# Performance work log

Measured on AMD Instinct MI355X. Metric: run time of the kernel, lower is better.

## Reference

```python
import jax, jax.numpy as jnp
import numpy as np

NEG_SLOPE = 0.01
EPS = 1e-5


def leaky_relu(x):
    return jnp.where(x >= 0, x, NEG_SLOPE * x)


def graph_conv(x, W, src, dst, edge_weight, num_nodes):
    # DGL GraphConv, norm='both', bias=False: D_out^{-1/2} A_w D_in^{-1/2} X W
    ones = jnp.ones_like(edge_weight)
    deg_out = jnp.maximum(jax.ops.segment_sum(ones, src, num_segments=num_nodes), 1.0)
    deg_in = jnp.maximum(jax.ops.segment_sum(ones, dst, num_segments=num_nodes), 1.0)
    h = x @ W
    h = h * jax.lax.rsqrt(deg_out)[:, None]
    agg = jax.ops.segment_sum(h[src] * edge_weight[:, None], dst, num_segments=num_nodes)
    return agg * jax.lax.rsqrt(deg_in)[:, None]


def graph_norm(x, alpha, gamma, beta, batch_size):
    # GraphNorm: per-graph, per-channel mean/var; graphs are equal-sized -> reshape
    n = x.shape[0] // batch_size
    xg = x.reshape(batch_size, n, x.shape[1])
    mean = xg.mean(axis=1, keepdims=True)
    sub = xg - alpha * mean
    var = (sub * sub).mean(axis=1, keepdims=True)
    out = gamma * sub * jax.lax.rsqrt(var + EPS) + beta
    return out.reshape(x.shape)


def instance_norm(x):
    # InstanceNorm1d (affine=False) on 2D input: per-row normalization over features
    mean = x.mean(axis=-1, keepdims=True)
    var = ((x - mean) ** 2).mean(axis=-1, keepdims=True)
    return (x - mean) * jax.lax.rsqrt(var + EPS)


def setup_inputs() -> dict:
    key = jax.random.key(0)
    ks = jax.random.split(key, 9)
    B, n = 4096, 64                      # graphs, nodes per graph (equal-sized)
    N = B * n                            # 262144 nodes
    E = 8 * N                            # avg degree 8
    in_feats, conv_dim, out_conv = 64, 128, 96
    in_mlp = out_conv * n                # 6144 = in_feats_mlp
    hid = 2048
    out_feats = 256

    def kaiming(k, fin, fout):
        bound = float(np.sqrt(6.0 / ((1 + NEG_SLOPE ** 2) * fin)))
        return jax.random.uniform(k, (fin, fout), jnp.float32, -bound, bound)

    def xavier(k, fin, fout):
        bound = float(np.sqrt(6.0 / (fin + fout)))
        return jax.random.uniform(k, (fin, fout), jnp.float32, -bound, bound)

    return {
        "x": jax.random.normal(ks[0], (N, in_feats), jnp.float32),
        "edge_weight": jax.random.uniform(ks[1], (E,), jnp.float32),
        "src": jax.random.randint(ks[2], (E,), 0, N, jnp.int32),
        "dst": jax.random.randint(ks[3], (E,), 0, N, jnp.int32),
        "W1": kaiming(ks[4], in_feats, conv_dim),
        "W2": kaiming(ks[5], conv_dim, out_conv),
        "gn1_alpha": jnp.ones((conv_dim,), jnp.float32),
        "gn1_gamma": jnp.ones((conv_dim,), jnp.float32),
        "gn1_beta": jnp.zeros((conv_dim,), jnp.float32),
        "gn2_alpha": jnp.ones((out_conv,), jnp.float32),
        "gn2_gamma": jnp.ones((out_conv,), jnp.float32),
        "gn2_beta": jnp.zeros((out_conv,), jnp.float32),
        "Win": xavier(ks[6], in_mlp, hid),
        "Whid": xavier(ks[7], hid, hid // 4),
        "Wcls": xavier(ks[8], hid // 4, out_feats),
        "batch_size": B,
    }


def reference(x, edge_weight, src, dst, W1, W2, gn1_alpha, gn1_gamma, gn1_beta,
              gn2_alpha, gn2_gamma, gn2_beta, Win, Whid, Wcls, batch_size):
    N = x.shape[0]
    h = graph_conv(x, W1, src, dst, edge_weight, N)
    h = leaky_relu(h)
    h = graph_norm(h, gn1_alpha, gn1_gamma, gn1_beta, batch_size)
    h = graph_conv(h, W2, src, dst, edge_weight, N)
    h = leaky_relu(h)
    h = graph_norm(h, gn2_alpha, gn2_gamma, gn2_beta, batch_size)
    # unbatch: each equal-size graph flattened to one row [B, n*out_conv]
    h = h.reshape(batch_size, -1)
    h = instance_norm(leaky_relu(h @ Win))   # dropout is identity (p=0 / eval)
    h = instance_norm(leaky_relu(h @ Whid))
    return h @ Wcls
```

## Files before the change

kernel.cpp:

```cpp
#include <hip/hip_runtime.h>
#include <hip/hip_bf16.h>

#define NN 262144
#define EE 2097152
#define BB 4096
constexpr int INMLP = 6144;
constexpr int HID = 2048;
constexpr int HID4 = 512;
constexpr int OUTF = 256;
constexpr int NSL = 64;
constexpr int ESL = EE / NSL;
constexpr int RNODES = 32768;

typedef short s16x8 __attribute__((ext_vector_type(8)));
typedef short s16x4 __attribute__((ext_vector_type(4)));
typedef float f32x4 __attribute__((ext_vector_type(4)));

__device__ __forceinline__ float lrelu(float v) { return v >= 0.f ? v : 0.01f * v; }
__device__ __forceinline__ float bf2f(short s) {
    unsigned int u = ((unsigned int)(unsigned short)s) << 16;
    return __builtin_bit_cast(float, u);
}
__device__ __forceinline__ short f2bf(float f) {
    unsigned int u = __builtin_bit_cast(unsigned int, f);
    u = (u + 0x7fff + ((u >> 16) & 1)) >> 16;
    return (short)u;
}
__device__ __forceinline__ void async16(const void* g, void* l) {
    __builtin_amdgcn_global_load_lds((__attribute__((address_space(1))) void*)g,
                                     (__attribute__((address_space(3))) void*)l, 16, 0, 0);
}

__global__ __launch_bounds__(256) void hist_count(const int* __restrict__ dst, const int* __restrict__ src,
                                                  unsigned* __restrict__ part_din, unsigned* __restrict__ part_dout,
                                                  unsigned short* __restrict__ rankpack16) {
    __shared__ unsigned hist[RNODES / 2];
    const int S = blockIdx.x & 63;
    const int R = (blockIdx.x >> 6) & 7;
    const int T = blockIdx.x >> 9;
    for (int i = threadIdx.x; i < RNODES / 2; i += 256) hist[i] = 0;
    __syncthreads();
    const int* idxarr = T ? src : dst;
    const int4* v4 = (const int4*)(idxarr + S * ESL);
#pragma unroll 4
    for (int i = 0; i < ESL / 4 / 256; i++) {
        const int q0 = i * 256 + threadIdx.x;
        int4 q = v4[q0];
        const int ebase = S * ESL + q0 * 4;
#pragma unroll
        for (int k = 0; k < 4; k++) {
            int idx = k == 0 ? q.x : k == 1 ? q.y : k == 2 ? q.z : q.w;
            if ((idx >> 15) == R) {
                int local = idx & (RNODES - 1);
                unsigned old = atomicAdd(&hist[local >> 1], 1u << ((local & 1) * 16));
                if (T == 0) {
                    unsigned rank = (old >> ((local & 1) * 16)) & 0xffffu;
                    rankpack16[ebase + k] = (unsigned short)((S << 10) | rank);
                }
            }
        }
    }
    __syncthreads();
    unsigned* dp = (T ? part_dout : part_din) + (size_t)S * (NN / 2) + R * (RNODES / 2);
    for (int i = threadIdx.x; i < RNODES / 2; i += 256) dp[i] = hist[i];
}

__global__ __launch_bounds__(256) void deg_reduce(const unsigned* __restrict__ part_din,
                                                  const unsigned* __restrict__ part_dout,
                                                  unsigned* __restrict__ repbase_w,
                                                  float* __restrict__ ro, float* __restrict__ ri,
                                                  int* __restrict__ din) {
    int i = blockIdx.x * 256 + threadIdx.x;
    unsigned runl = 0, runh = 0, dl = 0, dh = 0;
#pragma unroll 8
    for (int S = 0; S < NSL; S++) {
        repbase_w[(size_t)S * (NN / 2) + i] = (runl & 0xffffu) | (runh << 16);
        unsigned w = part_din[(size_t)S * (NN / 2) + i];
        runl += w & 0xffffu; runh += w >> 16;
        unsigned w2 = part_dout[(size_t)S * (NN / 2) + i];
        dl += w2 & 0xffffu; dh += w2 >> 16;
    }
    int n0 = 2 * i, n1 = 2 * i + 1;
    din[n0] = (int)runl; din[n1] = (int)runh;
    ro[n0] = rsqrtf((float)(dl < 1u ? 1u : dl));
    ro[n1] = rsqrtf((float)(dh < 1u ? 1u : dh));
    ri[n0] = rsqrtf((float)(runl < 1u ? 1u : runl));
    ri[n1] = rsqrtf((float)(runh < 1u ? 1u : runh));
}

__global__ __launch_bounds__(256) void scanA(const int* __restrict__ cnt, int* __restrict__ blks) {
    __shared__ int s[256];
    int t = threadIdx.x;
    int i0 = blockIdx.x * 1024 + t * 4;
    int ts = cnt[i0] + cnt[i0 + 1] + cnt[i0 + 2] + cnt[i0 + 3];
    s[t] = ts; __syncthreads();
    for (int d = 128; d > 0; d >>= 1) { if (t < d) s[t] += s[t + d]; __syncthreads(); }
    if (t == 0) blks[blockIdx.x] = s[0];
}

__global__ __launch_bounds__(256) void scanB(int* __restrict__ blks, int* __restrict__ offN) {
    __shared__ int s[256];
    int t = threadIdx.x;
    int v = blks[t]; s[t] = v; __syncthreads();
    for (int d = 1; d < 256; d <<= 1) {
        int x = (t >= d) ? s[t - d] : 0; __syncthreads();
        s[t] += x; __syncthreads();
    }
    blks[t] = s[t] - v;
    if (t == 255) *offN = s[255];
}

__global__ __launch_bounds__(256) void scanC(const int* __restrict__ cnt, const int* __restrict__ blkoff,
                                             int* __restrict__ off) {
    __shared__ int s[256];
    int t = threadIdx.x;
    int i0 = blockIdx.x * 1024 + t * 4;
    int v0 = cnt[i0], v1 = cnt[i0 + 1], v2 = cnt[i0 + 2], v3 = cnt[i0 + 3];
    int ts = v0 + v1 + v2 + v3;
    s[t] = ts; __syncthreads();
    for (int d = 1; d < 256; d <<= 1) {
        int x = (t >= d) ? s[t - d] : 0; __syncthreads();
        s[t] += x; __syncthreads();
    }
    int base = blkoff[blockIdx.x] + (s[t] - ts);
    off[i0] = base; off[i0 + 1] = base + v0; off[i0 + 2] = base + v0 + v1; off[i0 + 3] = base + v0 + v1 + v2;
}

__global__ __launch_bounds__(256) void fill_csr(const int* __restrict__ src, const int* __restrict__ dst,
                                                const float* __restrict__ ew, const float* __restrict__ ro,
                                                const int* __restrict__ off,
                                                const unsigned short* __restrict__ repbase16,
                                                const unsigned short* __restrict__ rankpack16,
                                                int2* __restrict__ edg) {
    int e = blockIdx.x * 256 + threadIdx.x;
    int d = dst[e];
    int s = src[e];
    unsigned pk = rankpack16[e];
    int S = pk >> 10, rank = pk & 1023;
    int p = off[d] + (int)repbase16[(size_t)S * NN + d] + rank;
    edg[p] = make_int2(s, __builtin_bit_cast(int, ew[e] * ro[s]));
}

__global__ __launch_bounds__(256) void cvt_x(const float* __restrict__ X, short* __restrict__ Xb) {
    int i = (blockIdx.x * 256 + threadIdx.x) * 4;
    float4 v = *(const float4*)(X + i);
    s16x4 o = { f2bf(v.x), f2bf(v.y), f2bf(v.z), f2bf(v.w) };
    *(s16x4*)(Xb + i) = o;
}

__global__ __launch_bounds__(256) void gather64(const short* __restrict__ Xb, const int* __restrict__ offs,
                                                const int2* __restrict__ edg, short* __restrict__ Out) {
    const int lane = threadIdx.x & 63;
    const int e = lane >> 3, c = lane & 7;
    int node = blockIdx.x * 4 + (threadIdx.x >> 6);
    node = __builtin_amdgcn_readfirstlane(node);
    const int s0 = offs[node], s1 = offs[node + 1];
    float acc[8] = {};
    for (int j0 = s0; j0 < s1; j0 += 8) {
        int j = j0 + e;
        bool ok = j < s1;
        int2 pe = edg[ok ? j : s0];
        int s = pe.x;
        float w = ok ? __builtin_bit_cast(float, pe.y) : 0.f;
        s16x8 v = *(const s16x8*)&Xb[(size_t)s * 64 + c * 8];
#pragma unroll
        for (int k = 0; k < 8; k++) acc[k] = fmaf(w, bf2f(v[k]), acc[k]);
    }
#pragma unroll
    for (int off = 8; off <= 32; off <<= 1)
#pragma unroll
        for (int k = 0; k < 8; k++) acc[k] += __shfl_xor(acc[k], off);
    if (e == 0) {
        s16x8 o;
#pragma unroll
        for (int k = 0; k < 8; k++) o[k] = f2bf(acc[k]);
        *(s16x8*)&Out[(size_t)node * 64 + c * 8] = o;
    }
}

__global__ __launch_bounds__(256) void gather96(const short* __restrict__ H, const int* __restrict__ offs,
                                                const int2* __restrict__ edg, short* __restrict__ Out) {
    const int lane = threadIdx.x & 63;
    const int e = lane >> 4, c = lane & 15;
    int node = blockIdx.x * 4 + (threadIdx.x >> 6);
    node = __builtin_amdgcn_readfirstlane(node);
    const int s0 = offs[node], s1 = offs[node + 1];
    float acc[6] = {};
    for (int j0 = s0; j0 < s1; j0 += 4) {
        int j = j0 + e;
        bool ok = j < s1;
        int2 pe = edg[ok ? j : s0];
        int s = pe.x;
        float w = ok ? __builtin_bit_cast(float, pe.y) : 0.f;
        const unsigned int* hp = (const unsigned int*)(H + (size_t)s * 96 + c * 6);
        unsigned int u0 = hp[0], u1 = hp[1], u2 = hp[2];
        acc[0] = fmaf(w, bf2f((short)(u0 & 0xffff)), acc[0]);
        acc[1] = fmaf(w, bf2f((short)(u0 >> 16)), acc[1]);
        acc[2] = fmaf(w, bf2f((short)(u1 & 0xffff)), acc[2]);
        acc[3] = fmaf(w, bf2f((short)(u1 >> 16)), acc[3]);
        acc[4] = fmaf(w, bf2f((short)(u2 & 0xffff)), acc[4]);
        acc[5] = fmaf(w, bf2f((short)(u2 >> 16)), acc[5]);
    }
#pragma unroll
    for (int off = 16; off <= 32; off <<= 1)
#pragma unroll
        for (int k = 0; k < 6; k++) acc[k] += __shfl_xor(acc[k], off);
    if (e == 0) {
        unsigned int* op = (unsigned int*)(Out + (size_t)node * 96 + c * 6);
        op[0] = (unsigned short)f2bf(acc[0]) | ((unsigned)(unsigned short)f2bf(acc[1]) << 16);
        op[1] = (unsigned short)f2bf(acc[2]) | ((unsigned)(unsigned short)f2bf(acc[3]) << 16);
        op[2] = (unsigned short)f2bf(acc[4]) | ((unsigned)(unsigned short)f2bf(acc[5]) << 16);
    }
}

template <int C>
__global__ __launch_bounds__(256) void graphnorm_k(short* __restrict__ Ag, const float* __restrict__ ri,
                                                   const float* __restrict__ alpha, const float* __restrict__ gamma,
                                                   const float* __restrict__ beta) {
    __shared__ float sm[64 * C];
    __shared__ float sscale[C], sshift[C];
    const int g = blockIdx.x;
    const size_t base = (size_t)g * 64 * C;
    for (int idx = threadIdx.x; idx < 64 * C; idx += 256) {
        int i = idx / C;
        float v = bf2f(Ag[base + idx]) * ri[g * 64 + i];
        sm[idx] = lrelu(v);
    }
    __syncthreads();
    if (threadIdx.x < C) {
        int c = threadIdx.x;
        float s1 = 0.f, s2 = 0.f;
#pragma unroll 4
        for (int i = 0; i < 64; i++) { float v = sm[i * C + c]; s1 += v; s2 += v * v; }
        float m = s1 * (1.f / 64.f);
        float a = alpha[c];
        float var = s2 * (1.f / 64.f) - m * m * a * (2.f - a);
        float sc = gamma[c] * rsqrtf(var + 1e-5f);
        sscale[c] = sc;
        sshift[c] = beta[c] - sc * a * m;
    }
    __syncthreads();
    for (int idx = threadIdx.x; idx < 64 * C; idx += 256) {
        int c = idx % C;
        Ag[base + idx] = f2bf(sscale[c] * sm[idx] + sshift[c]);
    }
}

__global__ __launch_bounds__(256) void conv1_gn(const short* __restrict__ A, const short* __restrict__ BT,
                                                const float* __restrict__ ri,
                                                const float* __restrict__ alpha, const float* __restrict__ gamma,
                                                const float* __restrict__ beta, short* __restrict__ Outp) {
    __shared__ short As[128][72];
    __shared__ short Bs[128][72];
    __shared__ float sscale[2][128], sshift[2][128];
    const int t = threadIdx.x;
    const int bm = blockIdx.x * 128;
    const int wave = t >> 6, lane = t & 63;
    const int wm = (wave & 1) * 64, wn = (wave >> 1) * 64;
    const int g = wave & 1;
    const int m16 = lane & 15, quad = lane >> 4;
#pragma unroll
    for (int i = 0; i < 4; i++) {
        int idx = t + 256 * i;
        int rr = idx >> 3, kk = (idx & 7) * 8;
        *(s16x8*)&As[rr][kk] = *(const s16x8*)&A[(size_t)(bm + rr) * 64 + kk];
        *(s16x8*)&Bs[rr][kk] = *(const s16x8*)&BT[(size_t)rr * 64 + kk];
    }
    __syncthreads();
    f32x4 acc[4][4] = {};
#pragma unroll
    for (int kc = 0; kc < 2; kc++) {
        s16x8 af[4], bfr[4];
#pragma unroll
        for (int mt = 0; mt < 4; mt++) af[mt] = *(const s16x8*)&As[wm + mt * 16 + m16][kc * 32 + quad * 8];
#pragma unroll
        for (int nt = 0; nt < 4; nt++) bfr[nt] = *(const s16x8*)&Bs[wn + nt * 16 + m16][kc * 32 + quad * 8];
#pragma unroll
        for (int mt = 0; mt < 4; mt++)
#pragma unroll
            for (int nt = 0; nt < 4; nt++)
                acc[mt][nt] = __builtin_amdgcn_mfma_f32_16x16x32_bf16(af[mt], bfr[nt], acc[mt][nt], 0, 0, 0);
    }
#pragma unroll
    for (int mt = 0; mt < 4; mt++)
#pragma unroll
        for (int r4 = 0; r4 < 4; r4++) {
            float rv = ri[bm + wm + mt * 16 + quad * 4 + r4];
#pragma unroll
            for (int nt = 0; nt < 4; nt++)
                acc[mt][nt][r4] = lrelu(acc[mt][nt][r4] * rv);
        }
#pragma unroll
    for (int nt = 0; nt < 4; nt++) {
        float s1 = 0.f, s2 = 0.f;
#pragma unroll
        for (int mt = 0; mt < 4; mt++)
#pragma unroll
            for (int r4 = 0; r4 < 4; r4++) { float v = acc[mt][nt][r4]; s1 += v; s2 += v * v; }
        s1 += __shfl_xor(s1, 16); s1 += __shfl_xor(s1, 32);
        s2 += __shfl_xor(s2, 16); s2 += __shfl_xor(s2, 32);
        if (quad == 0) {
            int ch = wn + nt * 16 + m16;
            float m = s1 * (1.f / 64.f);
            float a = alpha[ch];
            float var = s2 * (1.f / 64.f) - m * m * a * (2.f - a);
            float sc = gamma[ch] * rsqrtf(var + 1e-5f);
            sscale[g][ch] = sc;
            sshift[g][ch] = beta[ch] - sc * a * m;
        }
    }
    __syncthreads();
#pragma unroll
    for (int nt = 0; nt < 4; nt++) {
        int ch = wn + nt * 16 + m16;
        float sc = sscale[g][ch], sh = sshift[g][ch];
#pragma unroll
        for (int mt = 0; mt < 4; mt++)
#pragma unroll
            for (int r4 = 0; r4 < 4; r4++) {
                int row = bm + wm + mt * 16 + quad * 4 + r4;
                Outp[(size_t)row * 128 + ch] = f2bf(sc * acc[mt][nt][r4] + sh);
            }
    }
}

__global__ __launch_bounds__(256) void conv2_mfma(const short* __restrict__ A, const short* __restrict__ BT,
                                                  short* __restrict__ H) {
    __shared__ short As[128][136];
    __shared__ short Bs[96][136];
    const int t = threadIdx.x;
    const int bm = blockIdx.x * 128;
    const int wave = t >> 6, lane = t & 63;
    const int wm = (wave & 1) * 64, wn = (wave >> 1) * 48;
    const int m16 = lane & 15, quad = lane >> 4;
#pragma unroll
    for (int i = 0; i < 8; i++) {
        int idx = t + 256 * i;
        int rr = idx >> 4, kk = (idx & 15) * 8;
        *(s16x8*)&As[rr][kk] = *(const s16x8*)&A[(size_t)(bm + rr) * 128 + kk];
    }
#pragma unroll
    for (int i = 0; i < 6; i++) {
        int idx = t + 256 * i;
        int nr = idx >> 4, kk = (idx & 15) * 8;
        *(s16x8*)&Bs[nr][kk] = *(const s16x8*)&BT[(size_t)nr * 128 + kk];
    }
    __syncthreads();
    f32x4 acc[4][3] = {};
#pragma unroll
    for (int kc = 0; kc < 4; kc++) {
        s16x8 af[4], bfr[3];
#pragma unroll
        for (int mt = 0; mt < 4; mt++) af[mt] = *(const s16x8*)&As[wm + mt * 16 + m16][kc * 32 + quad * 8];
#pragma unroll
        for (int nt = 0; nt < 3; nt++) bfr[nt] = *(const s16x8*)&Bs[wn + nt * 16 + m16][kc * 32 + quad * 8];
#pragma unroll
        for (int mt = 0; mt < 4; mt++)
#pragma unroll
            for (int nt = 0; nt < 3; nt++)
                acc[mt][nt] = __builtin_amdgcn_mfma_f32_16x16x32_bf16(af[mt], bfr[nt], acc[mt][nt], 0, 0, 0);
    }
#pragma unroll
    for (int mt = 0; mt < 4; mt++)
#pragma unroll
        for (int r4 = 0; r4 < 4; r4++) {
            int row = bm + wm + mt * 16 + quad * 4 + r4;
#pragma unroll
            for (int nt = 0; nt < 3; nt++)
                H[(size_t)row * 96 + wn + nt * 16 + m16] = f2bf(acc[mt][nt][r4]);
        }
}

__global__ __launch_bounds__(256) void transp_cvt(const float* __restrict__ W, short* __restrict__ WT,
                                                  int R, int Cc) {
    __shared__ short tile[32][33];
    const int bc = blockIdx.x * 32;
    const int br = blockIdx.y * 32;
    const int tx = threadIdx.x & 31, ty = threadIdx.x >> 5;
#pragma unroll
    for (int i = 0; i < 32; i += 8)
        tile[ty + i][tx] = f2bf(W[(size_t)(br + ty + i) * Cc + bc + tx]);
    __syncthreads();
#pragma unroll
    for (int i = 0; i < 32; i += 8)
        WT[(size_t)(bc + ty + i) * R + br + tx] = tile[tx][ty + i];
}

#define MBAR() __builtin_amdgcn_s_barrier()
#define LGKM0() asm volatile("s_waitcnt lgkmcnt(0)" ::: "memory")
#define SB0() __builtin_amdgcn_sched_barrier(0)

__global__ __launch_bounds__(512, 2) void mlp1_mfma8(const short* __restrict__ A, const short* __restrict__ BT,
                                                     short* __restrict__ Cp) {
    constexpr int K = INMLP;
    __shared__ short As[2][256 * 64];
    __shared__ short Bs[2][256 * 64];
    const int t = threadIdx.x;
    const int wid = t >> 6, lane = t & 63;
    const int lrow = lane >> 3, lcol = lane & 7;
    const int scol = lcol ^ (lrow & 7);
    const int m16 = lane & 15, quad = lane >> 4, xkey = m16 & 7;
    const int wm = wid & 1, wn = wid >> 1;
    const int sw = (blockIdx.x & 7) * 32 + (blockIdx.x >> 3);
    const int bm = sw & 15, bn = (sw >> 4) & 7, z = sw >> 7;
    const short* gA = A + (size_t)(bm * 256 + wid * 32 + lrow) * K + (size_t)z * (K / 2) + scol * 8;
    const short* gB = BT + (size_t)(bn * 256 + wid * 16 + lrow) * K + (size_t)z * (K / 2) + scol * 8;

    s16x8 a0[8], a1[8], b0[4], b1[4];
    f32x4 acc[8][4] = {};

#define STAGE_A(s, ko) \
    { _Pragma("unroll") for (int j = 0; j < 4; j++) \
        async16(gA + (size_t)(j * 8) * K + (ko), &As[s][(wid * 32 + j * 8) * 64]); }
#define STAGE_B(s, ko, h) \
    { _Pragma("unroll") for (int j = 0; j < 2; j++) \
        async16(gB + (size_t)((h) * 128 + j * 8) * K + (ko), &Bs[s][((h) * 128 + wid * 16 + j * 8) * 64]); }
#define LD_A(s, kc, d) \
    { _Pragma("unroll") for (int mt = 0; mt < 8; mt++) \
        d[mt] = *(const s16x8*)&As[s][(wm * 128 + mt * 16 + m16) * 64 + (((kc) * 4 + quad) ^ xkey) * 8]; }
#define LD_B(s, kc, d) \
    { _Pragma("unroll") for (int nt = 0; nt < 4; nt++) \
        d[nt] = *(const s16x8*)&Bs[s][(wn * 64 + nt * 16 + m16) * 64 + (((kc) * 4 + quad) ^ xkey) * 8]; }
#define MM2(a, b, nlo) \
    { _Pragma("unroll") for (int mt = 0; mt < 8; mt++) { \
        acc[mt][(nlo)] = __builtin_amdgcn_mfma_f32_16x16x32_bf16(a[mt], b[(nlo)], acc[mt][(nlo)], 0, 0, 0); \
        acc[mt][(nlo) + 1] = __builtin_amdgcn_mfma_f32_16x16x32_bf16(a[mt], b[(nlo) + 1], acc[mt][(nlo) + 1], 0, 0, 0); } }

    STAGE_A(0, 0); STAGE_B(0, 0, 0); STAGE_B(0, 0, 1);
    STAGE_B(1, 64, 0); STAGE_B(1, 64, 1); STAGE_A(1, 64);
    asm volatile("s_waitcnt vmcnt(8)" ::: "memory");
    MBAR();

    int kof = 0;
#pragma unroll 1
    for (int i = 0; i < 24; i++, kof += 128) {
        const bool st = (i < 23);
        LD_A(0, 0, a0); LD_B(0, 0, b0);
        MBAR(); LGKM0(); SB0();
        __builtin_amdgcn_s_setprio(1); MM2(a0, b0, 0); __builtin_amdgcn_s_setprio(0);
        MBAR();
        LD_A(0, 1, a1); LD_B(0, 1, b1);
        MBAR(); LGKM0(); SB0();
        __builtin_amdgcn_s_setprio(1); MM2(a0, b0, 2); __builtin_amdgcn_s_setprio(0);
        MBAR();
        if (st) STAGE_A(0, kof + 128);
        MBAR(); LGKM0(); SB0();
        __builtin_amdgcn_s_setprio(1); MM2(a1, b1, 0); __builtin_amdgcn_s_setprio(0);
        if (st) { asm volatile("s_waitcnt vmcnt(4)" ::: "memory"); }
        else    { asm volatile("s_waitcnt vmcnt(0)" ::: "memory"); }
        MBAR();
        LD_A(1, 0, a0); LD_B(1, 0, b0);
        if (st) STAGE_B(0, kof + 128, 0);
        MBAR(); LGKM0(); SB0();
        __builtin_amdgcn_s_setprio(1); MM2(a1, b1, 2); __builtin_amdgcn_s_setprio(0);
        MBAR();
        LD_A(1, 1, a1); LD_B(1, 1, b1);
        if (st) STAGE_B(0, kof + 128, 1);
        MBAR(); LGKM0(); SB0();
        __builtin_amdgcn_s_setprio(1); MM2(a0, b0, 0); __builtin_amdgcn_s_setprio(0);
        MBAR();
        if (st) STAGE_B(1, kof + 192, 0);
        MBAR(); LGKM0(); SB0();
        __builtin_amdgcn_s_setprio(1); MM2(a0, b0, 2); __builtin_amdgcn_s_setprio(0);
        MBAR();
        if (st) STAGE_B(1, kof + 192, 1);
        MBAR(); LGKM0(); SB0();
        __builtin_amdgcn_s_setprio(1); MM2(a1, b1, 0); __builtin_amdgcn_s_setprio(0);
        MBAR();
        if (st) STAGE_A(1, kof + 192);
        MBAR(); LGKM0(); SB0();
        __builtin_amdgcn_s_setprio(1); MM2(a1, b1, 2); __builtin_amdgcn_s_setprio(0);
        if (st) { asm volatile("s_waitcnt vmcnt(8)" ::: "memory"); }
        MBAR();
    }

    short* C = Cp + (size_t)z * BB * HID;
    const int r0 = bm * 256 + wm * 128 + quad * 4;
    const int c0 = bn * 256 + wn * 64 + m16;
#pragma unroll
    for (int mt = 0; mt < 8; mt++)
#pragma unroll
        for (int nt = 0; nt < 4; nt++)
#pragma unroll
            for (int r4 = 0; r4 < 4; r4++)
                C[(size_t)(r0 + mt * 16 + r4) * HID + c0 + nt * 16] = f2bf(acc[mt][nt][r4]);
#undef STAGE_A
#undef STAGE_B
#undef LD_A
#undef LD_B
#undef MM2
}

__global__ __launch_bounds__(256) void rownorm_hid(short* __restrict__ D0, const short* __restrict__ D1) {
    const size_t base = (size_t)blockIdx.x * HID;
    float v[8];
    float s1 = 0.f, s2 = 0.f;
    const int c0 = threadIdx.x * 8;
    {
        s16x8 a = *(const s16x8*)&D0[base + c0];
        s16x8 b = *(const s16x8*)&D1[base + c0];
#pragma unroll
        for (int k = 0; k < 8; k++) {
            float x = lrelu(bf2f(a[k]) + bf2f(b[k]));
            v[k] = x; s1 += x; s2 += x * x;
        }
    }
#pragma unroll
    for (int o = 32; o > 0; o >>= 1) { s1 += __shfl_down(s1, o); s2 += __shfl_down(s2, o); }
    __shared__ float w1[4], w2[4];
    if ((threadIdx.x & 63) == 0) { w1[threadIdx.x >> 6] = s1; w2[threadIdx.x >> 6] = s2; }
    __syncthreads();
    s1 = w1[0] + w1[1] + w1[2] + w1[3];
    s2 = w2[0] + w2[1] + w2[2] + w2[3];
    float m = s1 * (1.f / HID);
    float inv = rsqrtf(s2 * (1.f / HID) - m * m + 1e-5f);
    s16x8 o;
#pragma unroll
    for (int k = 0; k < 8; k++) o[k] = f2bf((v[k] - m) * inv);
    *(s16x8*)&D0[base + c0] = o;
}

template <bool ABF16, bool LEAKY>
__global__ __launch_bounds__(256) void mfma_gemm(const float* __restrict__ Af, const short* __restrict__ Ab,
                                                 const short* __restrict__ BT,
                                                 float* __restrict__ C, int M, int Nn, int K) {
    __shared__ short As[64][40];
    __shared__ short Bs[64][40];
    const int t = threadIdx.x;
    const int bm = blockIdx.x * 64, bn = blockIdx.y * 64;
    const int wave = t >> 6, lane = t & 63;
    const int wm = (wave & 1) * 32, wn = (wave >> 1) * 32;
    const int m16 = lane & 15, quad = lane >> 4;
    const int rr = t >> 2, kk = (t & 3) * 8;
    f32x4 acc[2][2] = {};
    for (int k0 = 0; k0 < K; k0 += 32) {
        if (ABF16) {
            *(s16x8*)&As[rr][kk] = *(const s16x8*)&Ab[(size_t)(bm + rr) * K + k0 + kk];
        } else {
            const float* ap = &Af[(size_t)(bm + rr) * K + k0 + kk];
            float4 v0 = *(const float4*)ap;
            float4 v1 = *(const float4*)(ap + 4);
            s16x8 a8;
            a8[0] = f2bf(v0.x); a8[1] = f2bf(v0.y); a8[2] = f2bf(v0.z); a8[3] = f2bf(v0.w);
            a8[4] = f2bf(v1.x); a8[5] = f2bf(v1.y); a8[6] = f2bf(v1.z); a8[7] = f2bf(v1.w);
            *(s16x8*)&As[rr][kk] = a8;
        }
        *(s16x8*)&Bs[rr][kk] = *(const s16x8*)&BT[(size_t)(bn + rr) * K + k0 + kk];
        __syncthreads();
        s16x8 af[2], bfr[2];
#pragma unroll
        for (int mt = 0; mt < 2; mt++) af[mt] = *(const s16x8*)&As[wm + mt * 16 + m16][quad * 8];
#pragma unroll
        for (int nt = 0; nt < 2; nt++) bfr[nt] = *(const s16x8*)&Bs[wn + nt * 16 + m16][quad * 8];
#pragma unroll
        for (int mt = 0; mt < 2; mt++)
#pragma unroll
            for (int nt = 0; nt < 2; nt++)
                acc[mt][nt] = __builtin_amdgcn_mfma_f32_16x16x32_bf16(af[mt], bfr[nt], acc[mt][nt], 0, 0, 0);
        __syncthreads();
    }
#pragma unroll
    for (int mt = 0; mt < 2; mt++)
#pragma unroll
        for (int nt = 0; nt < 2; nt++)
#pragma unroll
            for (int r4 = 0; r4 < 4; r4++) {
                int row = bm + wm + mt * 16 + quad * 4 + r4;
                int col = bn + wn + nt * 16 + m16;
                float v = acc[mt][nt][r4];
                if (LEAKY) v = lrelu(v);
                C[(size_t)row * Nn + col] = v;
            }
}

template <int NC>
__global__ __launch_bounds__(256) void rownorm(float* __restrict__ Y) {
    float* p = Y + (size_t)blockIdx.x * NC;
    float s1 = 0.f, s2 = 0.f;
    for (int c = threadIdx.x; c < NC; c += 256) { float v = p[c]; s1 += v; s2 += v * v; }
#pragma unroll
    for (int o = 32; o > 0; o >>= 1) { s1 += __shfl_down(s1, o); s2 += __shfl_down(s2, o); }
    __shared__ float w1[4], w2[4];
    if ((threadIdx.x & 63) == 0) { w1[threadIdx.x >> 6] = s1; w2[threadIdx.x >> 6] = s2; }
    __syncthreads();
    s1 = w1[0] + w1[1] + w1[2] + w1[3];
    s2 = w2[0] + w2[1] + w2[2] + w2[3];
    float m = s1 * (1.f / NC);
    float inv = rsqrtf(s2 * (1.f / NC) - m * m + 1e-5f);
    for (int c = threadIdx.x; c < NC; c += 256) p[c] = (p[c] - m) * inv;
}

extern "C" void kernel_launch(void* const* d_in, const int* in_sizes, int n_in,
                              void* d_out, int out_size, void* d_ws, size_t ws_size,
                              hipStream_t stream) {
    const float* x    = (const float*)d_in[0];
    const float* ew   = (const float*)d_in[1];
    const int*   src  = (const int*)d_in[2];
    const int*   dst  = (const int*)d_in[3];
    const float* W1   = (const float*)d_in[4];
    const float* W2   = (const float*)d_in[5];
    const float* a1   = (const float*)d_in[6];
    const float* g1   = (const float*)d_in[7];
    const float* b1   = (const float*)d_in[8];
    const float* a2   = (const float*)d_in[9];
    const float* g2   = (const float*)d_in[10];
    const float* b2   = (const float*)d_in[11];
    const float* Win  = (const float*)d_in[12];
    const float* Whid = (const float*)d_in[13];
    const float* Wcls = (const float*)d_in[14];
    float* out = (float*)d_out;

    float* ro   = (float*)d_ws;
    float* ri   = ro + NN;
    int*   din  = (int*)(ri + NN);
    int*   offs = din + NN;
    int*   blks = offs + NN + 4;
    short* w1t  = (short*)(blks + 256);
    short* w2t  = w1t + 128 * 64;
    int2*  edg  = (int2*)(((size_t)(w2t + 96 * 128) + 15) & ~(size_t)15);
    short* Abf  = (short*)(edg + EE);
    short* Bbf  = Abf + (size_t)NN * 128;
    short* xbf  = Abf;
    short* aggx = Abf + (size_t)NN * 64;
    unsigned*       part_din   = (unsigned*)Abf;
    unsigned*       part_dout  = part_din + (size_t)NSL * (NN / 2);
    unsigned*       repbase_w  = (unsigned*)Bbf;
    unsigned short* rankpack16 = (unsigned short*)(repbase_w + (size_t)NSL * (NN / 2));
    short* WinT = Abf;
    short* D0   = (short*)((char*)Abf + 25165824);
    short* D1   = D0 + (size_t)BB * HID;
    float* Y2   = (float*)edg;
    short* WhidT = Bbf;
    short* WclsT = WhidT + (size_t)HID4 * HID;

    hist_count<<<2 * 8 * NSL, 256, 0, stream>>>(dst, src, part_din, part_dout, rankpack16);
    deg_reduce<<<NN / 512, 256, 0, stream>>>(part_din, part_dout, repbase_w, ro, ri, din);

    scanA<<<NN / 1024, 256, 0, stream>>>(din, blks);
    scanB<<<1, 256, 0, stream>>>(blks, offs + NN);
    scanC<<<NN / 1024, 256, 0, stream>>>(din, blks, offs);
    fill_csr<<<EE / 256, 256, 0, stream>>>(src, dst, ew, ro, offs,
                                           (const unsigned short*)repbase_w, rankpack16, edg);

    cvt_x<<<NN * 64 / 1024, 256, 0, stream>>>(x, xbf);
    transp_cvt<<<dim3(128 / 32, 64 / 32), 256, 0, stream>>>(W1, w1t, 64, 128);
    gather64<<<NN / 4, 256, 0, stream>>>(xbf, offs, edg, aggx);
    conv1_gn<<<NN / 128, 256, 0, stream>>>(aggx, w1t, ri, a1, g1, b1, Bbf);

    transp_cvt<<<dim3(96 / 32, 128 / 32), 256, 0, stream>>>(W2, w2t, 128, 96);
    conv2_mfma<<<NN / 128, 256, 0, stream>>>(Bbf, w2t, Abf);
    gather96<<<NN / 4, 256, 0, stream>>>(Abf, offs, edg, Bbf);
    graphnorm_k<96><<<BB, 256, 0, stream>>>(Bbf, ri, a2, g2, b2);

    transp_cvt<<<dim3(HID / 32, INMLP / 32), 256, 0, stream>>>(Win, WinT, INMLP, HID);
    mlp1_mfma8<<<256, 512, 0, stream>>>(Bbf, WinT, D0);
    transp_cvt<<<dim3(HID4 / 32, HID / 32), 256, 0, stream>>>(Whid, WhidT, HID, HID4);
    transp_cvt<<<dim3(OUTF / 32, HID4 / 32), 256, 0, stream>>>(Wcls, WclsT, HID4, OUTF);
    rownorm_hid<<<BB, 256, 0, stream>>>(D0, D1);
    mfma_gemm<true, true><<<dim3(BB / 64, HID4 / 64), 256, 0, stream>>>(nullptr, D0, WhidT, Y2, BB, HID4, HID);
    rownorm<HID4><<<BB, 256, 0, stream>>>(Y2);
    mfma_gemm<false, false><<<dim3(BB / 64, OUTF / 64), 256, 0, stream>>>(Y2, nullptr, WclsT, out, BB, OUTF, HID4);
}
```

Measured before the change: 944.7 us.

## Restructure MLP1 GEMM main loop into eight M-half phases with new staging schedule

Reorganizes the bf16 MFMA GEMM main loop so each phase loads a 4x4 fragment set (half of the M tiles) and runs 16 MFMAs, instead of loading full A/B fragments for two k-chunks. Global-to-LDS staging is regrouped into four-row-block batches per buffer, interleaved across phases with adjusted vmcnt waits. The aim is to cut register pressure from double fragment buffers and to spread memory traffic more evenly against compute. The cost is that B fragments are reloaded from LDS once per M-half, and the new wait counts must still match the staging order.

```diff
diff --git a/kernel.cpp b/kernel.cpp
--- a/kernel.cpp
+++ b/kernel.cpp
@@ -389,6 +389,9 @@
 #define MBAR() __builtin_amdgcn_s_barrier()
 #define LGKM0() asm volatile("s_waitcnt lgkmcnt(0)" ::: "memory")
 #define SB0() __builtin_amdgcn_sched_barrier(0)
+#define VMC4() asm volatile("s_waitcnt vmcnt(4)" ::: "memory")
+#define VMC2() asm volatile("s_waitcnt vmcnt(2)" ::: "memory")
+#define VMC0() asm volatile("s_waitcnt vmcnt(0)" ::: "memory")
 
 __global__ __launch_bounds__(512, 2) void mlp1_mfma8(const short* __restrict__ A, const short* __restrict__ BT,
                                                      short* __restrict__ Cp) {
@@ -403,74 +406,69 @@
     const int wm = wid & 1, wn = wid >> 1;
     const int sw = (blockIdx.x & 7) * 32 + (blockIdx.x >> 3);
     const int bm = sw & 15, bn = (sw >> 4) & 7, z = sw >> 7;
-    const short* gA = A + (size_t)(bm * 256 + wid * 32 + lrow) * K + (size_t)z * (K / 2) + scol * 8;
-    const short* gB = BT + (size_t)(bn * 256 + wid * 16 + lrow) * K + (size_t)z * (K / 2) + scol * 8;
-
-    s16x8 a0[8], a1[8], b0[4], b1[4];
+    const short* gA = A + (size_t)(bm * 256 + lrow) * K + (size_t)z * (K / 2) + scol * 8;
+    const short* gB = BT + (size_t)(bn * 256 + lrow) * K + (size_t)z * (K / 2) + scol * 8;
+
     f32x4 acc[8][4] = {};
 
-#define STAGE_A(s, ko) \
-    { _Pragma("unroll") for (int j = 0; j < 4; j++) \
-        async16(gA + (size_t)(j * 8) * K + (ko), &As[s][(wid * 32 + j * 8) * 64]); }
-#define STAGE_B(s, ko, h) \
-    { _Pragma("unroll") for (int j = 0; j < 2; j++) \
-        async16(gB + (size_t)((h) * 128 + j * 8) * K + (ko), &Bs[s][((h) * 128 + wid * 16 + j * 8) * 64]); }
-#define LD_A(s, kc, d) \
-    { _Pragma("unroll") for (int mt = 0; mt < 8; mt++) \
-        d[mt] = *(const s16x8*)&As[s][(wm * 128 + mt * 16 + m16) * 64 + (((kc) * 4 + quad) ^ xkey) * 8]; }
-#define LD_B(s, kc, d) \
-    { _Pragma("unroll") for (int nt = 0; nt < 4; nt++) \
-        d[nt] = *(const s16x8*)&Bs[s][(wn * 64 + nt * 16 + m16) * 64 + (((kc) * 4 + quad) ^ xkey) * 8]; }
-#define MM2(a, b, nlo) \
-    { _Pragma("unroll") for (int mt = 0; mt < 8; mt++) { \
-        acc[mt][(nlo)] = __builtin_amdgcn_mfma_f32_16x16x32_bf16(a[mt], b[(nlo)], acc[mt][(nlo)], 0, 0, 0); \
-        acc[mt][(nlo) + 1] = __builtin_amdgcn_mfma_f32_16x16x32_bf16(a[mt], b[(nlo) + 1], acc[mt][(nlo) + 1], 0, 0, 0); } }
-
-    STAGE_A(0, 0); STAGE_B(0, 0, 0); STAGE_B(0, 0, 1);
-    STAGE_B(1, 64, 0); STAGE_B(1, 64, 1); STAGE_A(1, 64);
-    asm volatile("s_waitcnt vmcnt(8)" ::: "memory");
+#define STG(gp, Xs, s, r0, ko) \
+    async16(gp + (size_t)((r0) + wid * 8) * K + (ko), &Xs[s][((r0) + wid * 8) * 64])
+#define STAGE_B4(s, ko) { STG(gB, Bs, s, 0, ko); STG(gB, Bs, s, 64, ko); STG(gB, Bs, s, 128, ko); STG(gB, Bs, s, 192, ko); }
+#define STAGE_A4(s, ko) { STG(gA, As, s, 0, ko); STG(gA, As, s, 128, ko); STG(gA, As, s, 64, ko); STG(gA, As, s, 192, ko); }
+#define PH_LOAD(s, kc, mh) \
+    { _Pragma("unroll") for (int mt = 0; mt < 4; mt++) \
+          af[mt] = *(const s16x8*)&As[s][(wm * 128 + (mh) * 64 + mt * 16 + m16) * 64 + (((kc) * 4 + quad) ^ xkey) * 8]; \
+      _Pragma("unroll") for (int nt = 0; nt < 4; nt++) \
+          bfr[nt] = *(const s16x8*)&Bs[s][(wn * 64 + nt * 16 + m16) * 64 + (((kc) * 4 + quad) ^ xkey) * 8]; }
+#define PH_MM(mh) \
+    { _Pragma("unroll") for (int mt = 0; mt < 4; mt++) \
+          _Pragma("unroll") for (int nt = 0; nt < 4; nt++) \
+              acc[(mh) * 4 + mt][nt] = __builtin_amdgcn_mfma_f32_16x16x32_bf16(af[mt], bfr[nt], acc[(mh) * 4 + mt][nt], 0, 0, 0); }
+
+    STAGE_B4(0, 0); STAGE_A4(0, 0);
+    VMC2();
     MBAR();
 
     int kof = 0;
 #pragma unroll 1
     for (int i = 0; i < 24; i++, kof += 128) {
         const bool st = (i < 23);
-        LD_A(0, 0, a0); LD_B(0, 0, b0);
-        MBAR(); LGKM0(); SB0();
-        __builtin_amdgcn_s_setprio(1); MM2(a0, b0, 0); __builtin_amdgcn_s_setprio(0);
+        s16x8 af[4], bfr[4];
+        PH_LOAD(0, 0, 0); STAGE_B4(1, kof + 64);
+        MBAR(); LGKM0(); SB0();
+        __builtin_amdgcn_s_setprio(1); PH_MM(0); __builtin_amdgcn_s_setprio(0);
+        VMC4(); MBAR();
+        PH_LOAD(0, 0, 1); STAGE_A4(1, kof + 64);
+        MBAR(); LGKM0(); SB0();
+        __builtin_amdgcn_s_setprio(1); PH_MM(1); __builtin_amdgcn_s_setprio(0);
         MBAR();
-        LD_A(0, 1, a1); LD_B(0, 1, b1);
-        MBAR(); LGKM0(); SB0();
-        __builtin_amdgcn_s_setprio(1); MM2(a0, b0, 2); __builtin_amdgcn_s_setprio(0);
+        PH_LOAD(0, 1, 0);
+        MBAR(); LGKM0(); SB0();
+        __builtin_amdgcn_s_setprio(1); PH_MM(0); __builtin_amdgcn_s_setprio(0);
         MBAR();
-        if (st) STAGE_A(0, kof + 128);
-        MBAR(); LGKM0(); SB0();
-        __builtin_amdgcn_s_setprio(1); MM2(a1, b1, 0); __builtin_amdgcn_s_setprio(0);
-        if (st) { asm volatile("s_waitcnt vmcnt(4)" ::: "memory"); }
-        else    { asm volatile("s_waitcnt vmcnt(0)" ::: "memory"); }
+        PH_LOAD(0, 1, 1);
+        MBAR(); LGKM0(); SB0();
+        __builtin_amdgcn_s_setprio(1); PH_MM(1); __builtin_amdgcn_s_setprio(0);
+        VMC2(); MBAR();
+        PH_LOAD(1, 0, 0);
+        if (st) STAGE_B4(0, kof + 128);
+        MBAR(); LGKM0(); SB0();
+        __builtin_amdgcn_s_setprio(1); PH_MM(0); __builtin_amdgcn_s_setprio(0);
+        if (st) { VMC4(); } else { VMC0(); }
         MBAR();
-        LD_A(1, 0, a0); LD_B(1, 0, b0);
-        if (st) STAGE_B(0, kof + 128, 0);
-        MBAR(); LGKM0(); SB0();
-        __builtin_amdgcn_s_setprio(1); MM2(a1, b1, 2); __builtin_amdgcn_s_setprio(0);
+        PH_LOAD(1, 0, 1);
+        if (st) STAGE_A4(0, kof + 128);
+        MBAR(); LGKM0(); SB0();
+        __builtin_amdgcn_s_setprio(1); PH_MM(1); __builtin_amdgcn_s_setprio(0);
         MBAR();
-        LD_A(1, 1, a1); LD_B(1, 1, b1);
-        if (st) STAGE_B(0, kof + 128, 1);
-        MBAR(); LGKM0(); SB0();
-        __builtin_amdgcn_s_setprio(1); MM2(a0, b0, 0); __builtin_amdgcn_s_setprio(0);
+        PH_LOAD(1, 1, 0);
+        MBAR(); LGKM0(); SB0();
+        __builtin_amdgcn_s_setprio(1); PH_MM(0); __builtin_amdgcn_s_setprio(0);
         MBAR();
-        if (st) STAGE_B(1, kof + 192, 0);
-        MBAR(); LGKM0(); SB0();
-        __builtin_amdgcn_s_setprio(1); MM2(a0, b0, 2); __builtin_amdgcn_s_setprio(0);
-        MBAR();
-        if (st) STAGE_B(1, kof + 192, 1);
-        MBAR(); LGKM0(); SB0();
-        __builtin_amdgcn_s_setprio(1); MM2(a1, b1, 0); __builtin_amdgcn_s_setprio(0);
-        MBAR();
-        if (st) STAGE_A(1, kof + 192);
-        MBAR(); LGKM0(); SB0();
-        __builtin_amdgcn_s_setprio(1); MM2(a1, b1, 2); __builtin_amdgcn_s_setprio(0);
-        if (st) { asm volatile("s_waitcnt vmcnt(8)" ::: "memory"); }
+        PH_LOAD(1, 1, 1);
+        MBAR(); LGKM0(); SB0();
+        __builtin_amdgcn_s_setprio(1); PH_MM(1); __builtin_amdgcn_s_setprio(0);
+        if (st) { VMC2(); }
         MBAR();
     }
 
@@ -484,11 +482,11 @@
 #pragma unroll
             for (int r4 = 0; r4 < 4; r4++)
                 C[(size_t)(r0 + mt * 16 + r4) * HID + c0 + nt * 16] = f2bf(acc[mt][nt][r4]);
-#undef STAGE_A
-#undef STAGE_B
-#undef LD_A
-#undef LD_B
-#undef MM2
+#undef STG
+#undef STAGE_A4
+#undef STAGE_B4
+#undef PH_LOAD
+#undef PH_MM
 }
 
 __global__ __launch_bounds__(256) void rownorm_hid(short* __restrict__ D0, const short* __restrict__ D1) {
```

New measurement: 797.3 us. 15.6% less time.
